# Performance work log

Hardware: AMD Instinct MI355X
Metric: run time of the kernel (lower is better)

Reference implementation:

```python
import jax, jax.numpy as jnp
import numpy as np
from jax import lax

EPS = 1e-6

def _instance_norm(x):
    # torch: std over flattened spatial, unbiased (ddof=1), + 1e-6
    b, c = x.shape[:2]
    xf = x.reshape(b, c, -1)
    mean = xf.mean(axis=2)[:, :, None, None]
    std = (jnp.std(xf, axis=2, ddof=1) + EPS)[:, :, None, None]
    return (x - mean) / std

def _conv1x1(x, w, b):
    # w: [O, I], x: [B, I, H, W]
    return jnp.einsum('oi,bihw->bohw', w, x) + b[None, :, None, None]

def _adaattn(content, style, ckey, skey, fw, fb, gw, gb, hw, hb):
    F = _conv1x1(ckey, fw, fb)   # [b, Ck, hc, wc]
    G = _conv1x1(skey, gw, gb)   # [b, Ck, hs, ws]
    H = _conv1x1(style, hw, hb)  # [b, Cv, hs, ws]
    b_, Ck, hc, wc = F.shape
    hs, ws = G.shape[2], G.shape[3]
    Fq = F.reshape(b_, Ck, hc * wc).transpose(0, 2, 1)   # [b, Nc, Ck]
    Gk = G.reshape(b_, Ck, hs * ws)                      # [b, Ck, Ns]
    Vs = H.reshape(b_, -1, hs * ws).transpose(0, 2, 1)   # [b, Ns, Cv]
    # Ns == hs*ws <= max_sample (4096) for these shapes -> no subsampling branch
    S = jax.nn.softmax(jnp.einsum('bnc,bcm->bnm', Fq, Gk), axis=-1)  # [b, Nc, Ns]
    mean = jnp.einsum('bnm,bmv->bnv', S, Vs)              # attention-weighted mean
    ex2 = jnp.einsum('bnm,bmv->bnv', S, Vs * Vs)          # E[x^2]
    std = jnp.sqrt(jax.nn.relu(ex2 - mean * mean))        # sqrt(relu(E[x^2]-E[x]^2))
    mean = mean.reshape(b_, hc, wc, -1).transpose(0, 3, 1, 2)
    std = std.reshape(b_, hc, wc, -1).transpose(0, 3, 1, 2)
    return std * _instance_norm(content) + mean

def _upsample2(x):
    return jnp.repeat(jnp.repeat(x, 2, axis=2), 2, axis=3)

def _conv3x3_reflect(x, w, b):
    xp = jnp.pad(x, ((0, 0), (0, 0), (1, 1), (1, 1)), mode='reflect')
    y = lax.conv_general_dilated(xp, w, window_strides=(1, 1), padding='VALID',
                                 dimension_numbers=('NCHW', 'OIHW', 'NCHW'))
    return y + b[None, :, None, None]


def setup_inputs() -> dict:
    key = jax.random.key(0)
    ks = jax.random.split(key, 16)
    f32 = jnp.float32
    d = {}
    d['content4_1'] = jax.random.normal(ks[0], (1, 512, 128, 128), f32)
    d['style4_1'] = jax.random.normal(ks[1], (1, 512, 64, 64), f32)
    d['content5_1'] = jax.random.normal(ks[2], (1, 512, 64, 64), f32)
    d['style5_1'] = jax.random.normal(ks[3], (1, 512, 32, 32), f32)
    d['content4_1_key'] = jax.random.normal(ks[4], (1, 960, 128, 128), f32)
    d['style4_1_key'] = jax.random.normal(ks[5], (1, 960, 64, 64), f32)
    d['content5_1_key'] = jax.random.normal(ks[6], (1, 1472, 64, 64), f32)
    d['style5_1_key'] = jax.random.normal(ks[7], (1, 1472, 32, 32), f32)
    def w2(k, o, i):
        return jax.random.normal(k, (o, i), f32) / np.sqrt(i).astype(np.float32)
    d['f4_w'] = w2(ks[8], 960, 960); d['f4_b'] = jnp.zeros((960,), f32)
    d['g4_w'] = w2(ks[9], 960, 960); d['g4_b'] = jnp.zeros((960,), f32)
    d['h4_w'] = w2(ks[10], 512, 512); d['h4_b'] = jnp.zeros((512,), f32)
    d['f5_w'] = w2(ks[11], 1472, 1472); d['f5_b'] = jnp.zeros((1472,), f32)
    d['g5_w'] = w2(ks[12], 1472, 1472); d['g5_b'] = jnp.zeros((1472,), f32)
    d['h5_w'] = w2(ks[13], 512, 512); d['h5_b'] = jnp.zeros((512,), f32)
    d['conv_w'] = jax.random.normal(ks[14], (512, 512, 3, 3), f32) / np.sqrt(512 * 9).astype(np.float32)
    d['conv_b'] = jnp.zeros((512,), f32)
    return d


def reference(content4_1, style4_1, content5_1, style5_1,
              content4_1_key, style4_1_key, content5_1_key, style5_1_key,
              f4_w, f4_b, g4_w, g4_b, h4_w, h4_b,
              f5_w, f5_b, g5_w, g5_b, h5_w, h5_b,
              conv_w, conv_b):
    a4 = _adaattn(content4_1, style4_1, content4_1_key, style4_1_key,
                  f4_w, f4_b, g4_w, g4_b, h4_w, h4_b)
    a5 = _adaattn(content5_1, style5_1, content5_1_key, style5_1_key,
                  f5_w, f5_b, g5_w, g5_b, h5_w, h5_b)
    return _conv3x3_reflect(a4 + _upsample2(a5), conv_w, conv_b)
```

## Files before the change

### kernel.cpp

```cpp
#include <hip/hip_runtime.h>
#include <math.h>


typedef _Float16 half8 __attribute__((ext_vector_type(8)));
typedef _Float16 half4 __attribute__((ext_vector_type(4)));
typedef float f32x4 __attribute__((ext_vector_type(4)));

__device__ __forceinline__ void async16(const void* g, void* lds) {
    __builtin_amdgcn_global_load_lds(
        (const __attribute__((address_space(1))) void*)g,
        (__attribute__((address_space(3))) void*)lds, 16, 0, 0);
}

__device__ inline float wave_sum64(float v) {
#pragma unroll
    for (int o = 32; o > 0; o >>= 1) v += __shfl_xor(v, o, 64);
    return v;
}

__global__ __launch_bounds__(256, 2) void mgemm_hl(
    const _Float16* __restrict__ Ahi, const _Float16* __restrict__ Alo,
    const _Float16* __restrict__ Bhi, const _Float16* __restrict__ Blo,
    float* __restrict__ Cf, int K, int lda, int ldb, int ldc,
    size_t splitStride) {
    __shared__ _Float16 Ash[4096], Asl[4096], Bsh[4096], Bsl[4096];
    const int t = threadIdx.x, wave = t >> 6, lane = t & 63;
    const int bm = blockIdx.y * 128, bn = blockIdx.x * 128;
    const int kbase = blockIdx.z * K;
    const int wr = (wave >> 1) * 64, wc = (wave & 1) * 64;
    const int lq = lane >> 4, lr = lane & 15;
    const int srow = wave * 32 + (lane >> 2);
    const int scolg = (lane & 3) ^ ((lane >> 3) & 3);

    f32x4 acc[4][4] = {};

    const size_t aoff = ((size_t)(bm + srow) * lda + kbase) * 2 + scolg * 16;
    const size_t boff = ((size_t)(bn + srow) * ldb + kbase) * 2 + scolg * 16;
    const char* pAh = (const char*)Ahi + aoff;
    const char* pAl = (const char*)Alo + aoff;
    const char* pBh = (const char*)Bhi + boff;
    const char* pBl = (const char*)Blo + boff;
    const size_t ar = (size_t)16 * lda * 2, br = (size_t)16 * ldb * 2;
    _Float16* dAh = Ash + wave * 1024;
    _Float16* dAl = Asl + wave * 1024;
    _Float16* dBh = Bsh + wave * 1024;
    _Float16* dBl = Bsl + wave * 1024;
    const int key = (lr >> 1) & 3;

    for (int k0 = 0; k0 < K; k0 += 32) {
        __syncthreads();
        async16(pAh, dAh);
        async16(pAh + ar, dAh + 512);
        async16(pAl, dAl);
        async16(pAl + ar, dAl + 512);
        async16(pBh, dBh);
        async16(pBh + br, dBh + 512);
        async16(pBl, dBl);
        async16(pBl + br, dBl + 512);
        pAh += 64;
        pAl += 64;
        pBh += 64;
        pBl += 64;
        __syncthreads();

        half8 ah[4], al[4], bh[4], bl[4];
#pragma unroll
        for (int i = 0; i < 4; i++) {
            const int ro = (wr + i * 16 + lr) * 32 + ((lq ^ key) * 8);
            ah[i] = *(const half8*)&Ash[ro];
            al[i] = *(const half8*)&Asl[ro];
        }
#pragma unroll
        for (int j = 0; j < 4; j++) {
            const int ro = (wc + j * 16 + lr) * 32 + ((lq ^ key) * 8);
            bh[j] = *(const half8*)&Bsh[ro];
            bl[j] = *(const half8*)&Bsl[ro];
        }
#pragma unroll
        for (int i = 0; i < 4; i++)
#pragma unroll
            for (int j = 0; j < 4; j++) {
                acc[i][j] = __builtin_amdgcn_mfma_f32_16x16x32_f16(
                    ah[i], bl[j], acc[i][j], 0, 0, 0);
                acc[i][j] = __builtin_amdgcn_mfma_f32_16x16x32_f16(
                    al[i], bh[j], acc[i][j], 0, 0, 0);
                acc[i][j] = __builtin_amdgcn_mfma_f32_16x16x32_f16(
                    ah[i], bh[j], acc[i][j], 0, 0, 0);
            }
    }
    float* Co = Cf + (size_t)blockIdx.z * splitStride;
#pragma unroll
    for (int i = 0; i < 4; i++) {
        const int m0 = bm + wr + i * 16 + lq * 4;
#pragma unroll
        for (int j = 0; j < 4; j++) {
            const int n = bn + wc + j * 16 + lr;
#pragma unroll
            for (int r = 0; r < 4; r++)
                Co[(size_t)(m0 + r) * ldc + n] = acc[i][j][r];
        }
    }
}

template <int BIAS_MODE, int OUT_MODE, bool CONV>
__global__ __launch_bounds__(256, 2) void mgemm16(
    const _Float16* __restrict__ A, const _Float16* __restrict__ B,
    const float* __restrict__ bias, float* __restrict__ Cf,
    _Float16* __restrict__ Ch, int K, int lda, int ldb, int ldc,
    size_t splitStride) {
    __shared__ _Float16 As[128 * 32];
    __shared__ _Float16 Bs[128 * 32];
    const int t = threadIdx.x, wave = t >> 6, lane = t & 63;
    const int bm = blockIdx.y * 128, bn = blockIdx.x * 128;
    const int kbase = blockIdx.z * K;
    const int wr = (wave >> 1) * 64, wc = (wave & 1) * 64;
    const int lq = lane >> 4, lr = lane & 15;
    const int srow = wave * 32 + (lane >> 2);
    const int scolg = (lane & 3) ^ ((lane >> 3) & 3);

    f32x4 acc[4][4] = {};

    const char* Ap = (const char*)A +
                     ((size_t)(bm + srow) * lda + kbase) * 2 + scolg * 16;
    const char* Bp = (const char*)B +
                     ((size_t)(bn + srow) * ldb + kbase) * 2 + scolg * 16;
    const size_t Astep = (size_t)16 * lda * 2;
    const size_t Bstep = (size_t)16 * ldb * 2;
    _Float16* As0 = &As[(wave * 32) * 32];
    _Float16* As1 = &As[(wave * 32 + 16) * 32];
    _Float16* Bs0 = &Bs[(wave * 32) * 32];
    _Float16* Bs1 = &Bs[(wave * 32 + 16) * 32];
    const int key = (lr >> 1) & 3;

    for (int k0 = 0; k0 < K; k0 += 32) {
        __syncthreads();
        async16(Ap, As0);
        async16(Ap + Astep, As1);
        if (CONV) {
            const int kg = kbase + k0;
            const int rI = kg >> 9;
            const int dy = rI / 3, dx = rI - 3 * dy;
            const int ci0 = kg & 511;
            const char* Bc =
                (const char*)B +
                (((size_t)(blockIdx.x + dy) * 130 + srow + dx) * 512 + ci0) * 2 +
                scolg * 16;
            async16(Bc, Bs0);
            async16(Bc + (size_t)16 * 512 * 2, Bs1);
        } else {
            async16(Bp, Bs0);
            async16(Bp + Bstep, Bs1);
            Bp += 64;
        }
        Ap += 64;
        __syncthreads();

        half8 af[4], bf[4];
#pragma unroll
        for (int i = 0; i < 4; i++)
            af[i] = *(const half8*)&As[(wr + i * 16 + lr) * 32 + (lq ^ key) * 8];
#pragma unroll
        for (int j = 0; j < 4; j++)
            bf[j] = *(const half8*)&Bs[(wc + j * 16 + lr) * 32 + (lq ^ key) * 8];
#pragma unroll
        for (int i = 0; i < 4; i++)
#pragma unroll
            for (int j = 0; j < 4; j++)
                acc[i][j] = __builtin_amdgcn_mfma_f32_16x16x32_f16(
                    af[i], bf[j], acc[i][j], 0, 0, 0);
    }

    float* Co = (OUT_MODE == 0) ? Cf + (size_t)blockIdx.z * splitStride : nullptr;
#pragma unroll
    for (int i = 0; i < 4; i++) {
        const int m0 = bm + wr + i * 16 + lq * 4;
#pragma unroll
        for (int j = 0; j < 4; j++) {
            const int n = bn + wc + j * 16 + lr;
#pragma unroll
            for (int r = 0; r < 4; r++) {
                const int m = m0 + r;
                float v = acc[i][j][r];
                if (BIAS_MODE == 2) v += bias[m];
                if (OUT_MODE == 0) {
                    Co[(size_t)m * ldc + n] = v;
                } else {
                    Ch[(size_t)m * ldc + n] = (_Float16)v;
                    Ch[(size_t)(m + 512) * ldc + n] = (_Float16)(v * v);
                }
            }
        }
    }
}

__global__ __launch_bounds__(256) void combine_hilo(
    const float* __restrict__ part, _Float16* __restrict__ hi,
    _Float16* __restrict__ lo, int nz, size_t zs) {
    size_t i = (size_t)blockIdx.x * 256 + threadIdx.x;
    float s = 0.f;
    for (int z = 0; z < nz; z++) s += part[z * zs + i];
    _Float16 h = (_Float16)s;
    hi[i] = h;
    lo[i] = (_Float16)(s - (float)h);
}

__global__ __launch_bounds__(256) void transpose_hilo(
    const float* __restrict__ src, _Float16* __restrict__ dsthi,
    _Float16* __restrict__ dstlo, long srcld, int dstld, int nvalid,
    int cvalid) {
    __shared__ float tile[32][33];
    const int t = threadIdx.x, tx = t & 31, ty = t >> 5;
    const int n0 = blockIdx.x * 32, c0 = blockIdx.y * 32;
    const int n = n0 + tx;
#pragma unroll
    for (int i = 0; i < 4; i++) {
        int c = c0 + ty + i * 8;
        tile[ty + i * 8][tx] =
            (c < cvalid && n < nvalid) ? src[(size_t)c * srcld + n] : 0.f;
    }
    __syncthreads();
#pragma unroll
    for (int i = 0; i < 4; i++) {
        int nn = ty + i * 8;
        float v = tile[tx][nn];
        _Float16 h = (_Float16)v;
        size_t o = (size_t)(n0 + nn) * dstld + c0 + tx;
        dsthi[o] = h;
        dstlo[o] = (_Float16)(v - (float)h);
    }
}

__global__ __launch_bounds__(256) void transpose_cvt16(
    const float* __restrict__ src, _Float16* __restrict__ dst, long srcld,
    int dstld) {
    __shared__ float tile[32][33];
    const int t = threadIdx.x, tx = t & 31, ty = t >> 5;
    const int n0 = blockIdx.x * 32, c0 = blockIdx.y * 32;
#pragma unroll
    for (int i = 0; i < 4; i++)
        tile[ty + i * 8][tx] = src[(size_t)(c0 + ty + i * 8) * srcld + n0 + tx];
    __syncthreads();
#pragma unroll
    for (int i = 0; i < 4; i++) {
        int nn = ty + i * 8;
        dst[(size_t)(n0 + nn) * dstld + c0 + tx] = (_Float16)tile[tx][nn];
    }
}

__global__ __launch_bounds__(256) void cvt16(const float* __restrict__ src,
                                             _Float16* __restrict__ dst) {
    int i = blockIdx.x * 256 + threadIdx.x;
    dst[i] = (_Float16)src[i];
}

__global__ __launch_bounds__(256) void convw_perm(const float* __restrict__ src,
                                                  _Float16* __restrict__ dst) {
    int idx = blockIdx.x * 256 + threadIdx.x;
    int o = idx / 4608, rem = idx - o * 4608;
    int r = rem >> 9, ci = rem & 511;
    dst[idx] = (_Float16)src[(size_t)o * 4608 + ci * 9 + r];
}

__global__ __launch_bounds__(256) void fold_vec(
    const float* __restrict__ mat, const float* __restrict__ vec,
    const float* __restrict__ addc, float* __restrict__ outv, int C, int Nout,
    long ldm) {
    __shared__ float red[4][64];
    const int t = threadIdx.x, lane = t & 63, seg = t >> 6;
    const int n = blockIdx.x * 64 + lane;
    const int chunk = (C + 3) >> 2;
    const int start = seg * chunk;
    const int end = min(C, start + chunk);
    float s0 = 0.f, s1 = 0.f, s2 = 0.f, s3 = 0.f;
    if (n < Nout) {
        int c = start;
        for (; c + 3 < end; c += 4) {
            s0 = fmaf(vec[c], mat[(size_t)c * ldm + n], s0);
            s1 = fmaf(vec[c + 1], mat[(size_t)(c + 1) * ldm + n], s1);
            s2 = fmaf(vec[c + 2], mat[(size_t)(c + 2) * ldm + n], s2);
            s3 = fmaf(vec[c + 3], mat[(size_t)(c + 3) * ldm + n], s3);
        }
        for (; c < end; c++) s0 = fmaf(vec[c], mat[(size_t)c * ldm + n], s0);
    }
    red[seg][lane] = (s0 + s1) + (s2 + s3);
    __syncthreads();
    if (seg == 0 && n < Nout)
        outv[n] = red[0][lane] + red[1][lane] + red[2][lane] + red[3][lane] +
                  (addc ? addc[0] : 0.f);
}

__global__ __launch_bounds__(256) void dotbb(const float* __restrict__ a,
                                             const float* __restrict__ b,
                                             float* __restrict__ out, int C) {
    __shared__ float red[4];
    const int t = threadIdx.x;
    float s = 0.f;
    for (int c = t; c < C; c += 256) s = fmaf(a[c], b[c], s);
    s = wave_sum64(s);
    if ((t & 63) == 0) red[t >> 6] = s;
    __syncthreads();
    if (t == 0) out[0] = red[0] + red[1] + red[2] + red[3];
}

template <int NPER, int NZ>
__global__ __launch_bounds__(256) void softmax2(const float* __restrict__ L,
                                                const float* __restrict__ rr,
                                                _Float16* __restrict__ S,
                                                size_t zs) {
    constexpr int NV = NPER / 4;
    __shared__ float redm[4], reds[4];
    const int t = threadIdx.x;
    const float* p = L + (size_t)blockIdx.x * (NPER * 256);
    _Float16* q = S + (size_t)blockIdx.x * (NPER * 256);
    f32x4 v[NV];
    float m = -3.0e38f;
#pragma unroll
    for (int i = 0; i < NV; i++) {
        const int c = t * 4 + i * 1024;
        f32x4 x = *(const f32x4*)(p + c);
        if (NZ == 2) x = x + *(const f32x4*)(p + zs + c);
        x = x + *(const f32x4*)(rr + c);
        v[i] = x;
        m = fmaxf(m, fmaxf(fmaxf(x[0], x[1]), fmaxf(x[2], x[3])));
    }
#pragma unroll
    for (int o = 32; o > 0; o >>= 1) m = fmaxf(m, __shfl_xor(m, o, 64));
    if ((t & 63) == 0) redm[t >> 6] = m;
    __syncthreads();
    m = fmaxf(fmaxf(redm[0], redm[1]), fmaxf(redm[2], redm[3]));
    float s = 0.f;
#pragma unroll
    for (int i = 0; i < NV; i++) {
        f32x4 x = v[i];
#pragma unroll
        for (int j = 0; j < 4; j++) {
            x[j] = __expf(x[j] - m);
            s += x[j];
        }
        v[i] = x;
    }
    s = wave_sum64(s);
    if ((t & 63) == 0) reds[t >> 6] = s;
    __syncthreads();
    const float inv = 1.f / (reds[0] + reds[1] + reds[2] + reds[3]);
#pragma unroll
    for (int i = 0; i < NV; i++) {
        const int c = t * 4 + i * 1024;
        half4 h;
#pragma unroll
        for (int j = 0; j < 4; j++) h[j] = (_Float16)(v[i][j] * inv);
        *(half4*)(q + c) = h;
    }
}

__global__ __launch_bounds__(256) void chanstats_kernel(
    const float* __restrict__ x, float* __restrict__ cm,
    float* __restrict__ cstd, int N) {
    __shared__ float rs[4], rs2[4];
    const int t = threadIdx.x;
    const float* p = x + (size_t)blockIdx.x * N;
    float s = 0.f, s2 = 0.f;
    for (int i = t; i < N; i += 256) {
        float v = p[i];
        s += v;
        s2 = fmaf(v, v, s2);
    }
    s = wave_sum64(s);
    s2 = wave_sum64(s2);
    if ((t & 63) == 0) {
        rs[t >> 6] = s;
        rs2[t >> 6] = s2;
    }
    __syncthreads();
    if (t == 0) {
        float S = rs[0] + rs[1] + rs[2] + rs[3];
        float S2 = rs2[0] + rs2[1] + rs2[2] + rs2[3];
        float mean = S / N;
        float var = fmaxf((S2 - S * mean) / (N - 1), 0.f);
        cm[blockIdx.x] = mean;
        cstd[blockIdx.x] = sqrtf(var) + 1e-6f;
    }
}

__global__ __launch_bounds__(256) void epilogue5(
    const float* __restrict__ pv, const float* __restrict__ content,
    const float* __restrict__ cm, const float* __restrict__ cstd,
    _Float16* __restrict__ a5t) {
    int idx = blockIdx.x * 256 + threadIdx.x;
    int n = idx >> 9, c = idx & 511;
    const size_t SS = (size_t)4096 * 1024;
    float mean = pv[(size_t)n * 1024 + c] + pv[SS + (size_t)n * 1024 + c];
    float ex2 =
        pv[(size_t)n * 1024 + 512 + c] + pv[SS + (size_t)n * 1024 + 512 + c];
    float sd = sqrtf(fmaxf(ex2 - mean * mean, 0.f));
    float cn = (content[(size_t)c * 4096 + n] - cm[c]) / cstd[c];
    a5t[idx] = (_Float16)(fmaf(sd, cn, mean));
}

__global__ __launch_bounds__(256) void epilogue4(
    const float* __restrict__ part, const float* __restrict__ content,
    const float* __restrict__ cm, const float* __restrict__ cstd,
    const _Float16* __restrict__ a5t, _Float16* __restrict__ pad4t, int n0) {
    int idx = blockIdx.x * 256 + threadIdx.x;
    int r = idx >> 9, c = idx & 511;
    int n = n0 + r;
    const size_t SS = (size_t)1024 * 1024;
    float mean = 0.f, ex2 = 0.f;
#pragma unroll
    for (int z = 0; z < 8; z++) {
        mean += part[z * SS + (size_t)r * 1024 + c];
        ex2 += part[z * SS + (size_t)r * 1024 + 512 + c];
    }
    float sd = sqrtf(fmaxf(ex2 - mean * mean, 0.f));
    float cn = (content[(size_t)c * 16384 + n] - cm[c]) / cstd[c];
    int y = n >> 7, x = n & 127;
    float up = (float)a5t[(size_t)((y >> 1) * 64 + (x >> 1)) * 512 + c];
    pad4t[(size_t)((y + 1) * 130 + (x + 1)) * 512 + c] =
        (_Float16)(fmaf(sd, cn, mean) + up);
}

__global__ __launch_bounds__(256) void border_kernel(_Float16* __restrict__ pad) {
    int idx = blockIdx.x * 256 + threadIdx.x;
    int pos = idx >> 9, c = idx & 511;
    int py, px;
    if (pos < 130) { py = 0; px = pos; }
    else if (pos < 260) { py = 129; px = pos - 130; }
    else if (pos < 388) { py = pos - 260 + 1; px = 0; }
    else { py = pos - 388 + 1; px = 129; }
    int sy = py == 0 ? 2 : (py == 129 ? 127 : py);
    int sx = px == 0 ? 2 : (px == 129 ? 127 : px);
    pad[(size_t)(py * 130 + px) * 512 + c] =
        pad[(size_t)(sy * 130 + sx) * 512 + c];
}


extern "C" void kernel_launch(void* const* d_in, const int* in_sizes, int n_in,
                              void* d_out, int out_size, void* d_ws,
                              size_t ws_size, hipStream_t stream) {
    (void)in_sizes; (void)n_in; (void)out_size; (void)ws_size;
    const float* content4 = (const float*)d_in[0];
    const float* style4 = (const float*)d_in[1];
    const float* content5 = (const float*)d_in[2];
    const float* style5 = (const float*)d_in[3];
    const float* ckey4 = (const float*)d_in[4];
    const float* skey4 = (const float*)d_in[5];
    const float* ckey5 = (const float*)d_in[6];
    const float* skey5 = (const float*)d_in[7];
    const float* f4w = (const float*)d_in[8];
    const float* f4b = (const float*)d_in[9];
    const float* g4w = (const float*)d_in[10];
    const float* g4b = (const float*)d_in[11];
    const float* h4w = (const float*)d_in[12];
    const float* h4b = (const float*)d_in[13];
    const float* f5w = (const float*)d_in[14];
    const float* f5b = (const float*)d_in[15];
    const float* g5w = (const float*)d_in[16];
    const float* g5b = (const float*)d_in[17];
    const float* h5w = (const float*)d_in[18];
    const float* h5b = (const float*)d_in[19];
    const float* convw = (const float*)d_in[20];
    const float* convb = (const float*)d_in[21];
    float* out = (float*)d_out;
    char* ws = (char*)d_ws;

    _Float16* PAD4T = (_Float16*)(ws + 0);
    _Float16* A5T = (_Float16*)(ws + 17305600);
    float* STATS = (float*)(ws + 21499904);
    _Float16* H4W = (_Float16*)(ws + 21508096);
    _Float16* H5W = (_Float16*)(ws + 22032384);
    _Float16* CONVW = (_Float16*)(ws + 22556672);
    float* U5 = (float*)(ws + 27275264);
    float* R5 = (float*)(ws + 27283456);
    float* U4 = (float*)(ws + 27291648);
    float* R4 = (float*)(ws + 27299840);
    float* BB5 = (float*)(ws + 27316224);
    float* BB4 = (float*)(ws + 27316480);
    char* A0 = ws + 27320320;

    float* cm4 = STATS, *cstd4 = STATS + 512, *cm5 = STATS + 1024,
         *cstd5 = STATS + 1536;

    chanstats_kernel<<<512, 256, 0, stream>>>(content5, cm5, cstd5, 4096);
    chanstats_kernel<<<512, 256, 0, stream>>>(content4, cm4, cstd4, 16384);
    cvt16<<<1024, 256, 0, stream>>>(h4w, H4W);
    cvt16<<<1024, 256, 0, stream>>>(h5w, H5W);
    convw_perm<<<9216, 256, 0, stream>>>(convw, CONVW);

    {
        _Float16* STT5 = (_Float16*)(A0 + 0);
        _Float16* HCAT5 = (_Float16*)(A0 + 1048576);
        _Float16* T5h = (_Float16*)(A0 + 3145728);
        _Float16* T5l = (_Float16*)(A0 + 6291456);
        _Float16* FWh = (_Float16*)(A0 + 9437184);
        _Float16* FWl = (_Float16*)(A0 + 14155776);
        _Float16* GWh = (_Float16*)(A0 + 18874368);
        _Float16* GWl = (_Float16*)(A0 + 23592960);
        float* PM5 = (float*)(A0 + 28311552);
        _Float16* M5h = (_Float16*)(A0 + 56623104);
        _Float16* M5l = (_Float16*)(A0 + 61341696);
        _Float16* SKh = (_Float16*)(A0 + 9437184);
        _Float16* SKl = (_Float16*)(A0 + 12582912);
        float* PT5 = (float*)(A0 + 15728640);
        _Float16* CKh = (_Float16*)(A0 + 9437184);
        _Float16* CKl = (_Float16*)(A0 + 22020096);
        float* LOG5 = (float*)(A0 + 34603008);
        _Float16* S5 = (_Float16*)(A0 + 9437184);

        dotbb<<<1, 256, 0, stream>>>(f5b, g5b, BB5, 1472);
        fold_vec<<<23, 256, 0, stream>>>(g5w, f5b, nullptr, U5, 1472, 1472, 1472);
        fold_vec<<<16, 256, 0, stream>>>(skey5, U5, BB5, R5, 1472, 1024, 1024);

        transpose_hilo<<<dim3(48, 48), 256, 0, stream>>>(f5w, FWh, FWl, 1472,
                                                         1536, 1472, 1472);
        transpose_hilo<<<dim3(48, 48), 256, 0, stream>>>(g5w, GWh, GWl, 1472,
                                                         1536, 1472, 1472);
        mgemm_hl<<<dim3(12, 12, 3), 256, 0, stream>>>(
            FWh, FWl, GWh, GWl, PM5, 512, 1536, 1536, 1536,
            (size_t)1536 * 1536);
        combine_hilo<<<9216, 256, 0, stream>>>(PM5, M5h, M5l, 3,
                                               (size_t)1536 * 1536);
        transpose_hilo<<<dim3(32, 48), 256, 0, stream>>>(skey5, SKh, SKl, 1024,
                                                         1536, 1024, 1472);
        mgemm_hl<<<dim3(12, 8, 3), 256, 0, stream>>>(
            SKh, SKl, M5h, M5l, PT5, 512, 1536, 1536, 1536,
            (size_t)1024 * 1536);
        combine_hilo<<<6144, 256, 0, stream>>>(PT5, T5h, T5l, 3,
                                               (size_t)1024 * 1536);
        transpose_cvt16<<<dim3(32, 16), 256, 0, stream>>>(style5, STT5, 1024, 512);
        mgemm16<2, 2, false><<<dim3(8, 4), 256, 0, stream>>>(
            H5W, STT5, h5b, nullptr, HCAT5, 512, 512, 512, 1024, 0);
        transpose_hilo<<<dim3(128, 48), 256, 0, stream>>>(ckey5, CKh, CKl, 4096,
                                                          1536, 4096, 1472);
        mgemm_hl<<<dim3(8, 32, 2), 256, 0, stream>>>(
            CKh, CKl, T5h, T5l, LOG5, 768, 1536, 1536, 1024,
            (size_t)4096 * 1024);
        softmax2<4, 2><<<4096, 256, 0, stream>>>(LOG5, R5, S5,
                                                 (size_t)4096 * 1024);
        mgemm16<0, 0, false><<<dim3(8, 32, 2), 256, 0, stream>>>(
            S5, HCAT5, nullptr, LOG5, nullptr, 512, 1024, 1024, 1024,
            (size_t)4096 * 1024);
        epilogue5<<<8192, 256, 0, stream>>>(LOG5, content5, cm5, cstd5, A5T);
    }

    {
        _Float16* T4h = (_Float16*)(A0 + 0);
        _Float16* T4l = (_Float16*)(A0 + 8388608);
        _Float16* M4h = (_Float16*)(A0 + 16777216);
        _Float16* M4l = (_Float16*)(A0 + 18874368);
        _Float16* FWh = (_Float16*)(A0 + 20971520);
        _Float16* FWl = (_Float16*)(A0 + 23068672);
        _Float16* GWh = (_Float16*)(A0 + 25165824);
        _Float16* GWl = (_Float16*)(A0 + 27262976);
        float* PM4 = (float*)(A0 + 29360128);
        _Float16* SKh = (_Float16*)(A0 + 20971520);
        _Float16* SKl = (_Float16*)(A0 + 29360128);
        float* PT4 = (float*)(A0 + 37748736);
        _Float16* HCAT4 = (_Float16*)(A0 + 16777216);
        _Float16* STT4 = (_Float16*)(A0 + 25165824);
        _Float16* CKh = (_Float16*)(A0 + 29360128);
        _Float16* CKl = (_Float16*)(A0 + 31457280);
        _Float16* S4 = (_Float16*)(A0 + 25165824);
        float* LOGR = (float*)(A0 + 33554432);

        dotbb<<<1, 256, 0, stream>>>(f4b, g4b, BB4, 960);
        fold_vec<<<15, 256, 0, stream>>>(g4w, f4b, nullptr, U4, 960, 960, 960);
        fold_vec<<<64, 256, 0, stream>>>(skey4, U4, BB4, R4, 960, 4096, 4096);

        transpose_hilo<<<dim3(32, 32), 256, 0, stream>>>(f4w, FWh, FWl, 960,
                                                         1024, 960, 960);
        transpose_hilo<<<dim3(32, 32), 256, 0, stream>>>(g4w, GWh, GWl, 960,
                                                         1024, 960, 960);
        mgemm_hl<<<dim3(8, 8, 4), 256, 0, stream>>>(
            FWh, FWl, GWh, GWl, PM4, 256, 1024, 1024, 1024,
            (size_t)1024 * 1024);
        combine_hilo<<<4096, 256, 0, stream>>>(PM4, M4h, M4l, 4,
                                               (size_t)1024 * 1024);
        transpose_hilo<<<dim3(128, 32), 256, 0, stream>>>(skey4, SKh, SKl, 4096,
                                                          1024, 4096, 960);
        mgemm_hl<<<dim3(8, 32, 2), 256, 0, stream>>>(
            SKh, SKl, M4h, M4l, PT4, 512, 1024, 1024, 1024,
            (size_t)4096 * 1024);
        combine_hilo<<<16384, 256, 0, stream>>>(PT4, T4h, T4l, 2,
                                                (size_t)4096 * 1024);
        transpose_cvt16<<<dim3(128, 16), 256, 0, stream>>>(style4, STT4, 4096, 512);
        mgemm16<2, 2, false><<<dim3(32, 4), 256, 0, stream>>>(
            H4W, STT4, h4b, nullptr, HCAT4, 512, 512, 512, 4096, 0);

        for (int chunk = 0; chunk < 16; chunk++) {
            const int n0 = chunk * 1024;
            transpose_hilo<<<dim3(32, 32), 256, 0, stream>>>(
                ckey4 + n0, CKh, CKl, 16384, 1024, 1024, 960);
            mgemm_hl<<<dim3(32, 8, 2), 256, 0, stream>>>(
                CKh, CKl, T4h, T4l, LOGR, 512, 1024, 1024, 4096,
                (size_t)1024 * 4096);
            softmax2<16, 2><<<1024, 256, 0, stream>>>(LOGR, R4, S4,
                                                      (size_t)1024 * 4096);
            mgemm16<0, 0, false><<<dim3(8, 8, 8), 256, 0, stream>>>(
                S4, HCAT4, nullptr, LOGR, nullptr, 512, 4096, 4096, 1024,
                (size_t)1024 * 1024);
            epilogue4<<<2048, 256, 0, stream>>>(LOGR, content4, cm4, cstd4, A5T,
                                                PAD4T, n0);
        }
    }

    border_kernel<<<1032, 256, 0, stream>>>(PAD4T);
    mgemm16<2, 0, true><<<dim3(128, 4), 256, 0, stream>>>(
        CONVW, PAD4T, convb, out, nullptr, 4608, 4608, 512, 16384, 0);
}
```

Measured before the change: 1.993 ms.

## Double the GEMM K-step per barrier and stagger block start times

```diff
diff --git a/kernel.cpp b/kernel.cpp
--- a/kernel.cpp
+++ b/kernel.cpp
@@ -10,6 +10,12 @@
     __builtin_amdgcn_global_load_lds(
         (const __attribute__((address_space(1))) void*)g,
         (__attribute__((address_space(3))) void*)lds, 16, 0, 0);
+}
+
+__device__ __forceinline__ void desync_sleep() {
+    const int lin =
+        blockIdx.x + gridDim.x * (blockIdx.y + gridDim.y * blockIdx.z);
+    if ((lin >> 8) & 1) __builtin_amdgcn_s_sleep(7);
 }
 
 __device__ inline float wave_sum64(float v) {
@@ -23,7 +29,7 @@
     const _Float16* __restrict__ Bhi, const _Float16* __restrict__ Blo,
     float* __restrict__ Cf, int K, int lda, int ldb, int ldc,
     size_t splitStride) {
-    __shared__ _Float16 Ash[4096], Asl[4096], Bsh[4096], Bsl[4096];
+    __shared__ _Float16 Ash[8192], Asl[8192], Bsh[8192], Bsl[8192];
     const int t = threadIdx.x, wave = t >> 6, lane = t & 63;
     const int bm = blockIdx.y * 128, bn = blockIdx.x * 128;
     const int kbase = blockIdx.z * K;
@@ -31,6 +37,8 @@
     const int lq = lane >> 4, lr = lane & 15;
     const int srow = wave * 32 + (lane >> 2);
     const int scolg = (lane & 3) ^ ((lane >> 3) & 3);
+
+    desync_sleep();
 
     f32x4 acc[4][4] = {};
 
@@ -47,7 +55,7 @@
     _Float16* dBl = Bsl + wave * 1024;
     const int key = (lr >> 1) & 3;
 
-    for (int k0 = 0; k0 < K; k0 += 32) {
+    for (int k0 = 0; k0 < K; k0 += 64) {
         __syncthreads();
         async16(pAh, dAh);
         async16(pAh + ar, dAh + 512);
@@ -57,36 +65,48 @@
         async16(pBh + br, dBh + 512);
         async16(pBl, dBl);
         async16(pBl + br, dBl + 512);
-        pAh += 64;
-        pAl += 64;
-        pBh += 64;
-        pBl += 64;
+        async16(pAh + 64, dAh + 4096);
+        async16(pAh + ar + 64, dAh + 4096 + 512);
+        async16(pAl + 64, dAl + 4096);
+        async16(pAl + ar + 64, dAl + 4096 + 512);
+        async16(pBh + 64, dBh + 4096);
+        async16(pBh + br + 64, dBh + 4096 + 512);
+        async16(pBl + 64, dBl + 4096);
+        async16(pBl + br + 64, dBl + 4096 + 512);
+        pAh += 128;
+        pAl += 128;
+        pBh += 128;
+        pBl += 128;
         __syncthreads();
 
-        half8 ah[4], al[4], bh[4], bl[4];
-#pragma unroll
-        for (int i = 0; i < 4; i++) {
-            const int ro = (wr + i * 16 + lr) * 32 + ((lq ^ key) * 8);
-            ah[i] = *(const half8*)&Ash[ro];
-            al[i] = *(const half8*)&Asl[ro];
-        }
-#pragma unroll
-        for (int j = 0; j < 4; j++) {
-            const int ro = (wc + j * 16 + lr) * 32 + ((lq ^ key) * 8);
-            bh[j] = *(const half8*)&Bsh[ro];
-            bl[j] = *(const half8*)&Bsl[ro];
-        }
-#pragma unroll
-        for (int i = 0; i < 4; i++)
+#pragma unroll
+        for (int s = 0; s < 2; s++) {
+            const int sb = s * 4096;
+            half8 ah[4], al[4], bh[4], bl[4];
+#pragma unroll
+            for (int i = 0; i < 4; i++) {
+                const int ro = sb + (wr + i * 16 + lr) * 32 + ((lq ^ key) * 8);
+                ah[i] = *(const half8*)&Ash[ro];
+                al[i] = *(const half8*)&Asl[ro];
+            }
 #pragma unroll
             for (int j = 0; j < 4; j++) {
-                acc[i][j] = __builtin_amdgcn_mfma_f32_16x16x32_f16(
-                    ah[i], bl[j], acc[i][j], 0, 0, 0);
-                acc[i][j] = __builtin_amdgcn_mfma_f32_16x16x32_f16(
-                    al[i], bh[j], acc[i][j], 0, 0, 0);
-                acc[i][j] = __builtin_amdgcn_mfma_f32_16x16x32_f16(
-                    ah[i], bh[j], acc[i][j], 0, 0, 0);
+                const int ro = sb + (wc + j * 16 + lr) * 32 + ((lq ^ key) * 8);
+                bh[j] = *(const half8*)&Bsh[ro];
+                bl[j] = *(const half8*)&Bsl[ro];
             }
+#pragma unroll
+            for (int i = 0; i < 4; i++)
+#pragma unroll
+                for (int j = 0; j < 4; j++) {
+                    acc[i][j] = __builtin_amdgcn_mfma_f32_16x16x32_f16(
+                        ah[i], bl[j], acc[i][j], 0, 0, 0);
+                    acc[i][j] = __builtin_amdgcn_mfma_f32_16x16x32_f16(
+                        al[i], bh[j], acc[i][j], 0, 0, 0);
+                    acc[i][j] = __builtin_amdgcn_mfma_f32_16x16x32_f16(
+                        ah[i], bh[j], acc[i][j], 0, 0, 0);
+                }
+        }
     }
     float* Co = Cf + (size_t)blockIdx.z * splitStride;
 #pragma unroll
@@ -108,8 +128,8 @@
     const float* __restrict__ bias, float* __restrict__ Cf,
     _Float16* __restrict__ Ch, int K, int lda, int ldb, int ldc,
     size_t splitStride) {
-    __shared__ _Float16 As[128 * 32];
-    __shared__ _Float16 Bs[128 * 32];
+    __shared__ _Float16 As[8192];
+    __shared__ _Float16 Bs[8192];
     const int t = threadIdx.x, wave = t >> 6, lane = t & 63;
     const int bm = blockIdx.y * 128, bn = blockIdx.x * 128;
     const int kbase = blockIdx.z * K;
@@ -118,6 +138,8 @@
     const int srow = wave * 32 + (lane >> 2);
     const int scolg = (lane & 3) ^ ((lane >> 3) & 3);
 
+    desync_sleep();
+
     f32x4 acc[4][4] = {};
 
     const char* Ap = (const char*)A +
@@ -126,48 +148,59 @@
                      ((size_t)(bn + srow) * ldb + kbase) * 2 + scolg * 16;
     const size_t Astep = (size_t)16 * lda * 2;
     const size_t Bstep = (size_t)16 * ldb * 2;
-    _Float16* As0 = &As[(wave * 32) * 32];
-    _Float16* As1 = &As[(wave * 32 + 16) * 32];
-    _Float16* Bs0 = &Bs[(wave * 32) * 32];
-    _Float16* Bs1 = &Bs[(wave * 32 + 16) * 32];
+    _Float16* As0 = As + wave * 1024;
+    _Float16* Bs0 = Bs + wave * 1024;
     const int key = (lr >> 1) & 3;
 
-    for (int k0 = 0; k0 < K; k0 += 32) {
+    for (int k0 = 0; k0 < K; k0 += 64) {
         __syncthreads();
         async16(Ap, As0);
-        async16(Ap + Astep, As1);
+        async16(Ap + Astep, As0 + 512);
+        async16(Ap + 64, As0 + 4096);
+        async16(Ap + Astep + 64, As0 + 4096 + 512);
         if (CONV) {
             const int kg = kbase + k0;
             const int rI = kg >> 9;
             const int dy = rI / 3, dx = rI - 3 * dy;
             const int ci0 = kg & 511;
-            const char* Bc =
-                (const char*)B +
-                (((size_t)(blockIdx.x + dy) * 130 + srow + dx) * 512 + ci0) * 2 +
-                scolg * 16;
+            const int py = (bn >> 7) + dy;
+            const int px = srow + dx;
+            const char* Bc = (const char*)B +
+                             (((size_t)py * 130 + px) * 512 + ci0) * 2 +
+                             scolg * 16;
             async16(Bc, Bs0);
-            async16(Bc + (size_t)16 * 512 * 2, Bs1);
+            async16(Bc + (size_t)16 * 512 * 2, Bs0 + 512);
+            async16(Bc + 64, Bs0 + 4096);
+            async16(Bc + (size_t)16 * 512 * 2 + 64, Bs0 + 4096 + 512);
         } else {
             async16(Bp, Bs0);
-            async16(Bp + Bstep, Bs1);
-            Bp += 64;
-        }
-        Ap += 64;
+            async16(Bp + Bstep, Bs0 + 512);
+            async16(Bp + 64, Bs0 + 4096);
+            async16(Bp + Bstep + 64, Bs0 + 4096 + 512);
+            Bp += 128;
+        }
+        Ap += 128;
         __syncthreads();
 
-        half8 af[4], bf[4];
-#pragma unroll
-        for (int i = 0; i < 4; i++)
-            af[i] = *(const half8*)&As[(wr + i * 16 + lr) * 32 + (lq ^ key) * 8];
-#pragma unroll
-        for (int j = 0; j < 4; j++)
-            bf[j] = *(const half8*)&Bs[(wc + j * 16 + lr) * 32 + (lq ^ key) * 8];
-#pragma unroll
-        for (int i = 0; i < 4; i++)
+#pragma unroll
+        for (int s = 0; s < 2; s++) {
+            const int sb = s * 4096;
+            half8 af[4], bf[4];
+#pragma unroll
+            for (int i = 0; i < 4; i++)
+                af[i] = *(const half8*)&As[sb + (wr + i * 16 + lr) * 32 +
+                                           (lq ^ key) * 8];
 #pragma unroll
             for (int j = 0; j < 4; j++)
-                acc[i][j] = __builtin_amdgcn_mfma_f32_16x16x32_f16(
-                    af[i], bf[j], acc[i][j], 0, 0, 0);
+                bf[j] = *(const half8*)&Bs[sb + (wc + j * 16 + lr) * 32 +
+                                           (lq ^ key) * 8];
+#pragma unroll
+            for (int i = 0; i < 4; i++)
+#pragma unroll
+                for (int j = 0; j < 4; j++)
+                    acc[i][j] = __builtin_amdgcn_mfma_f32_16x16x32_f16(
+                        af[i], bf[j], acc[i][j], 0, 0, 0);
+        }
     }
 
     float* Co = (OUT_MODE == 0) ? Cf + (size_t)blockIdx.z * splitStride : nullptr;
```

Measured after the change: 1.964 ms. Within noise of the previous version (-1.5%).
